# Kernel optimization log

Hardware: AMD Instinct MI355X
Metric: run time of the kernel (lower is better)

## Reference

```python
import jax, jax.numpy as jnp
import numpy as np

B = 32768
NMU = 3
K = 8
TMAX = 31.41592653589793
DE = 128
NC = 64
ZC = 1
IN_DIM = K + K * NMU  # 32

FREQS = jnp.asarray(1.0 / (np.float32(TMAX) ** np.arange(K // 2, dtype=np.float32)))


def _sinenc(x):
    # x: (B,) or (B,d) -> (B, K) or (B, d*K); per-feature [sin|cos] blocks concatenated
    if x.ndim == 1:
        xw = x[:, None] * FREQS[None, :]
        return jnp.concatenate([jnp.sin(xw), jnp.cos(xw)], axis=1)
    xw = x[:, :, None] * FREQS[None, None, :]  # (B, d, K/2)
    return jnp.concatenate([jnp.sin(xw), jnp.cos(xw)], axis=2).reshape(x.shape[0], -1)


def _conv3(x, w, b):
    y = jax.lax.conv_general_dilated(x, w, window_strides=(1, 1), padding=((1, 1), (1, 1)),
                                     dimension_numbers=("NCHW", "OIHW", "NCHW"))
    return y + b[None, :, None, None]


def setup_inputs() -> dict:
    key = jax.random.key(0)
    ks = jax.random.split(key, 20)
    s = 0.05
    return {
        "t": jax.random.uniform(ks[0], (B,), jnp.float32) * TMAX,
        "z": jax.random.normal(ks[1], (B, ZC, 4, 4), jnp.float32),
        "mu": jax.random.normal(ks[2], (B, NMU), jnp.float32),
        "W1": jax.random.normal(ks[3], (IN_DIM, DE), jnp.float32) * s,
        "b1": jnp.zeros((DE,), jnp.float32),
        "W2": jax.random.normal(ks[4], (DE, DE), jnp.float32) * s,
        "b2": jnp.zeros((DE,), jnp.float32),
        "Wg": jax.random.normal(ks[5], (DE, 4 * NC), jnp.float32) * s,
        "bg": jnp.zeros((4 * NC,), jnp.float32),
        "cin_w": jax.random.normal(ks[6], (NC, ZC, 3, 3), jnp.float32) * s,
        "cin_b": jnp.zeros((NC,), jnp.float32),
        "c1_w": jax.random.normal(ks[7], (NC, NC, 3, 3), jnp.float32) * s,
        "c1_b": jnp.zeros((NC,), jnp.float32),
        "c2_w": jax.random.normal(ks[8], (NC, NC, 3, 3), jnp.float32) * s,
        "c2_b": jnp.zeros((NC,), jnp.float32),
        "cout_w": jax.random.normal(ks[9], (ZC, NC, 3, 3), jnp.float32) * s,
        "cout_b": jnp.zeros((ZC,), jnp.float32),
    }


def reference(t, z, mu, W1, b1, W2, b2, Wg, bg,
              cin_w, cin_b, c1_w, c1_b, c2_w, c2_b, cout_w, cout_b):
    t_emb = _sinenc(t)            # (B, K)
    mu_emb = _sinenc(mu)          # (B, K*nmu)
    x = jnp.concatenate([t_emb, mu_emb], axis=1)  # (B, in_dim)
    h = jax.nn.elu(x @ W1 + b1)
    xi = jax.nn.elu(h @ W2 + b2)
    gb = (xi @ Wg + bg).reshape(-1, 4, NC)
    g1 = gb[:, 0][:, :, None, None]
    g2 = gb[:, 1][:, :, None, None]
    bb1 = gb[:, 2][:, :, None, None]
    bb2 = gb[:, 3][:, :, None, None]
    hh = jnp.tanh(_conv3(z, cin_w, cin_b))
    hh = jnp.tanh(g1 * _conv3(hh, c1_w, c1_b) + bb1)
    hh = jnp.tanh(g2 * _conv3(hh, c2_w, c2_b) + bb2)
    return _conv3(hh, cout_w, cout_b)
```

## Files before the change

### kernel.cpp

```cpp
#include <hip/hip_runtime.h>
#include <cstdint>
#include <cstddef>


#define NB 32768

typedef _Float16 half8   __attribute__((ext_vector_type(8)));
typedef _Float16 half4_t __attribute__((ext_vector_type(4)));
typedef _Float16 half2_t __attribute__((ext_vector_type(2)));
typedef float    f32x4   __attribute__((ext_vector_type(4)));

__device__ __forceinline__ float fast_tanh(float x) {
  float e = __expf(2.0f * x);
  return 1.0f - __fdividef(2.0f, e + 1.0f);
}

__device__ __forceinline__ float elu_f(float v) {
  return v > 0.0f ? v : (__expf(v) - 1.0f);
}

__device__ __forceinline__ void conv_acc(float acc[16], const float r[16], const float w[9]) {
#pragma unroll
  for (int y = 0; y < 4; ++y)
#pragma unroll
    for (int x = 0; x < 4; ++x)
#pragma unroll
      for (int ky = 0; ky < 3; ++ky) {
        int iy = y + ky - 1;
        if (iy < 0 || iy >= 4) continue;
#pragma unroll
        for (int kx = 0; kx < 3; ++kx) {
          int ix = x + kx - 1;
          if (ix < 0 || ix >= 4) continue;
          acc[y * 4 + x] += w[ky * 3 + kx] * r[iy * 4 + ix];
        }
      }
}

__global__ __launch_bounds__(256) void prep_kernel(
    const float* __restrict__ W1, const float* __restrict__ W2,
    const float* __restrict__ Wg, const float* __restrict__ c1w,
    const float* __restrict__ c2w, _Float16* __restrict__ wt) {
  int idx = blockIdx.x * 256 + threadIdx.x;
  _Float16* W1f = wt;
  _Float16* W2f = W1f + 4096;
  _Float16* Wgf = W2f + 16384;
  _Float16* c1t = Wgf + 32768;
  _Float16* c2t = c1t + 36864;
  if (idx < 4096) {
    int i = idx, j = i & 7, lane = (i >> 3) & 63, nt = i >> 9;
    int n = nt * 16 + (lane & 15), k = (lane >> 4) * 8 + j;
    W1f[i] = (_Float16)W1[k * 128 + n];
  } else if (idx < 20480) {
    int i = idx - 4096, j = i & 7, lane = (i >> 3) & 63, r = i >> 9;
    int kb = r & 3, nt = r >> 2;
    int n = nt * 16 + (lane & 15), k = kb * 32 + (lane >> 4) * 8 + j;
    W2f[i] = (_Float16)W2[k * 128 + n];
  } else if (idx < 53248) {
    int i = idx - 20480, j = i & 7, lane = (i >> 3) & 63, r = i >> 9;
    int kb = r & 3, ut = r >> 2;
    int n = ut * 16 + (lane & 15), k = kb * 32 + (lane >> 4) * 8 + j;
    Wgf[i] = (_Float16)Wg[k * 256 + n];
  } else if (idx < 90112) {
    int i = idx - 53248;
    int ts = i >> 11, r = i & 2047, oc = r >> 5, icw = r & 31;
    int tap = ts >> 1, kb = ts & 1, ic = kb * 32 + icw;
    c1t[i] = (_Float16)c1w[(oc * 64 + ic) * 9 + tap];
  } else if (idx < 126976) {
    int i = idx - 90112;
    int ts = i >> 11, r = i & 2047, oc = r >> 5, icw = r & 31;
    int tap = ts >> 1, kb = ts & 1, ic = kb * 32 + icw;
    c2t[i] = (_Float16)c2w[(oc * 64 + ic) * 9 + tap];
  }
}

#define ROWE 72
#define SAMP 2592
#define GS 4
#define GRPS 16
#define GBROW 264

__device__ __forceinline__ void mid_layer_mfma(
    const _Float16* __restrict__ src, _Float16* __restrict__ dst,
    const half8 af[18], const f32x4 cbv,
    const _Float16* __restrict__ gbase, int goff,
    int wv, int q, int py, int px) {
  f32x4 acc[GS];
#pragma unroll
  for (int g = 0; g < GS; ++g) acc[g] = (f32x4)(0.0f);
#pragma unroll
  for (int tap = 0; tap < 9; ++tap) {
    const int ky = tap / 3, kx = tap % 3;
    const int row = py + ky;
    const int pos = row * 6 + px + kx;
    const int e = (row ^ (pos >> 2)) & 1;
    const int o0 = pos * ROWE + q * 8 + e * 32;
    const int o1 = pos * ROWE + q * 8 + 32 - e * 32;
#pragma unroll
    for (int g = 0; g < GS; ++g) {
      half8 bb = *(const half8*)(src + g * SAMP + o0);
      acc[g] = __builtin_amdgcn_mfma_f32_16x16x32_f16(af[tap * 2 + 0], bb, acc[g], 0, 0, 0);
    }
#pragma unroll
    for (int g = 0; g < GS; ++g) {
      half8 bb = *(const half8*)(src + g * SAMP + o1);
      acc[g] = __builtin_amdgcn_mfma_f32_16x16x32_f16(af[tap * 2 + 1], bb, acc[g], 0, 0, 0);
    }
  }
  const int icb = wv * 16 + q * 4;
  const int row = 1 + py;
  const int pos = row * 6 + 1 + px;
  const int e = (row ^ (pos >> 2)) & 1;
  const int daddr = pos * ROWE + (((icb >> 5) ^ e) << 5) + (icb & 31);
#pragma unroll
  for (int g = 0; g < GS; ++g) {
    const _Float16* gp = gbase + g * GBROW + goff + icb;
    half4_t gv = *(const half4_t*)(gp);
    half4_t bv = *(const half4_t*)(gp + 128);
    half4_t o;
#pragma unroll
    for (int r = 0; r < 4; ++r)
      o[r] = (_Float16)fast_tanh((float)gv[r] * (acc[g][r] + cbv[r]) + (float)bv[r]);
    *(half4_t*)(dst + g * SAMP + daddr) = o;
  }
}

__global__ __launch_bounds__(256, 2) void fused_kernel(
    const float* __restrict__ tt, const float* __restrict__ mu,
    const float* __restrict__ z, const _Float16* __restrict__ wt,
    const float* __restrict__ b1, const float* __restrict__ b2,
    const float* __restrict__ bg,
    const float* __restrict__ cin_w, const float* __restrict__ cin_b,
    const float* __restrict__ c1_b, const float* __restrict__ c2_b,
    const float* __restrict__ cout_w, const float* __restrict__ cout_b,
    float* __restrict__ out) {
  const int tid = threadIdx.x;
  const int lane = tid & 63;
  const int wv = tid >> 6;
  const int m = lane & 15, q = lane >> 4, q8 = q * 8, q4 = q * 4;
  const int py = m >> 2, px = m & 3;
  const int s0 = blockIdx.x * (GRPS * GS);

  const _Float16* W1f = wt;
  const _Float16* W2f = W1f + 4096;
  const _Float16* Wgf = W2f + 16384;
  const _Float16* c1t = Wgf + 32768;
  const _Float16* c2t = c1t + 36864;

  __shared__ __align__(16) _Float16 hp[2 * GS * SAMP];
  __shared__ __align__(16) _Float16 gb_lds[64 * GBROW];
  __shared__ __align__(16) _Float16 cwl[9 * 64];

  {
    const int sl = wv * 16 + m;
    const int s = s0 + sl;
    _Float16* xw = hp + wv * SAMP;

    const float TM = 31.41592653589793f;
    float base = (q == 0) ? tt[s] : mu[(size_t)s * 3 + (q - 1)];
    half8 xb;
    float fr = 1.0f;
#pragma unroll
    for (int j = 0; j < 4; ++j) {
      float sn, cs;
      __sincosf(base * fr, &sn, &cs);
      xb[j] = (_Float16)sn;
      xb[4 + j] = (_Float16)cs;
      fr *= (1.0f / TM);
    }

#pragma unroll
    for (int nt = 0; nt < 8; ++nt) {
      half8 af = *(const half8*)(W1f + (nt * 64 + lane) * 8);
      f32x4 c = __builtin_amdgcn_mfma_f32_16x16x32_f16(af, xb, (f32x4)(0.0f), 0, 0, 0);
      f32x4 bv = *(const f32x4*)(b1 + nt * 16 + q4);
      half4_t o;
#pragma unroll
      for (int r = 0; r < 4; ++r) o[r] = (_Float16)elu_f(c[r] + bv[r]);
      *(half4_t*)(xw + m * 136 + nt * 16 + q4) = o;
    }
    half8 xf0 = *(const half8*)(xw + m * 136 + 0 + q8);
    half8 xf1 = *(const half8*)(xw + m * 136 + 32 + q8);
    half8 xf2 = *(const half8*)(xw + m * 136 + 64 + q8);
    half8 xf3 = *(const half8*)(xw + m * 136 + 96 + q8);

#pragma unroll
    for (int nt = 0; nt < 8; ++nt) {
      const _Float16* wp = W2f + (nt * 4) * 512 + lane * 8;
      f32x4 c = (f32x4)(0.0f);
      c = __builtin_amdgcn_mfma_f32_16x16x32_f16(*(const half8*)(wp), xf0, c, 0, 0, 0);
      c = __builtin_amdgcn_mfma_f32_16x16x32_f16(*(const half8*)(wp + 512), xf1, c, 0, 0, 0);
      c = __builtin_amdgcn_mfma_f32_16x16x32_f16(*(const half8*)(wp + 1024), xf2, c, 0, 0, 0);
      c = __builtin_amdgcn_mfma_f32_16x16x32_f16(*(const half8*)(wp + 1536), xf3, c, 0, 0, 0);
      f32x4 bv = *(const f32x4*)(b2 + nt * 16 + q4);
      half4_t o;
#pragma unroll
      for (int r = 0; r < 4; ++r) o[r] = (_Float16)elu_f(c[r] + bv[r]);
      *(half4_t*)(xw + m * 136 + nt * 16 + q4) = o;
    }
    half8 yf0 = *(const half8*)(xw + m * 136 + 0 + q8);
    half8 yf1 = *(const half8*)(xw + m * 136 + 32 + q8);
    half8 yf2 = *(const half8*)(xw + m * 136 + 64 + q8);
    half8 yf3 = *(const half8*)(xw + m * 136 + 96 + q8);

#pragma unroll
    for (int ut = 0; ut < 16; ++ut) {
      const _Float16* wp = Wgf + (ut * 4) * 512 + lane * 8;
      f32x4 c = (f32x4)(0.0f);
      c = __builtin_amdgcn_mfma_f32_16x16x32_f16(*(const half8*)(wp), yf0, c, 0, 0, 0);
      c = __builtin_amdgcn_mfma_f32_16x16x32_f16(*(const half8*)(wp + 512), yf1, c, 0, 0, 0);
      c = __builtin_amdgcn_mfma_f32_16x16x32_f16(*(const half8*)(wp + 1024), yf2, c, 0, 0, 0);
      c = __builtin_amdgcn_mfma_f32_16x16x32_f16(*(const half8*)(wp + 1536), yf3, c, 0, 0, 0);
      f32x4 bv = *(const f32x4*)(bg + ut * 16 + q4);
      half4_t o;
#pragma unroll
      for (int r = 0; r < 4; ++r) o[r] = (_Float16)(c[r] + bv[r]);
      *(half4_t*)(gb_lds + sl * GBROW + ut * 16 + q4) = o;
    }
  }

  half8 a1f[18], a2f[18];
#pragma unroll
  for (int t = 0; t < 18; ++t) {
    a1f[t] = *(const half8*)(c1t + t * 2048 + (wv * 16 + m) * 32 + q8);
    a2f[t] = *(const half8*)(c2t + t * 2048 + (wv * 16 + m) * 32 + q8);
  }
  float cw9[9];
#pragma unroll
  for (int t = 0; t < 9; ++t) cw9[t] = cin_w[lane * 9 + t];
  const float cinb = cin_b[lane];
  const float cob = cout_b[0];
  const f32x4 cb1 = *(const f32x4*)(c1_b + wv * 16 + q4);
  const f32x4 cb2 = *(const f32x4*)(c2_b + wv * 16 + q4);

  __syncthreads();

  for (int i = tid; i < (2 * GS * SAMP) / 2; i += 256) ((uint32_t*)hp)[i] = 0u;
  for (int i = tid; i < 576; i += 256) {
    int ic = i / 9, tap = i % 9;
    cwl[tap * 64 + ic] = (_Float16)cout_w[i];
  }
  __syncthreads();

  for (int grp = 0; grp < GRPS; ++grp) {
    const int sg = s0 + grp * GS;
    const _Float16* gbase = gb_lds + (size_t)(grp * GS) * GBROW;

    {
      const float* zp = z + (size_t)(sg + wv) * 16;
      float r[16], acc[16];
#pragma unroll
      for (int p = 0; p < 16; ++p) { r[p] = zp[p]; acc[p] = 0.0f; }
      conv_acc(acc, r, cw9);
      _Float16* dst = hp + wv * SAMP;
      const int ics = lane & 31, ich = lane >> 5;
#pragma unroll
      for (int p = 0; p < 16; ++p) {
        int row = 1 + (p >> 2);
        int pos = row * 6 + 1 + (p & 3);
        int e = (row ^ (pos >> 2)) & 1;
        dst[pos * ROWE + ((ich ^ e) << 5) + ics] = (_Float16)fast_tanh(acc[p] + cinb);
      }
    }
    __syncthreads();

    mid_layer_mfma(hp, hp + GS * SAMP, a1f, cb1, gbase, 0, wv, q, py, px);
    __syncthreads();

    mid_layer_mfma(hp + GS * SAMP, hp, a2f, cb2, gbase, 64, wv, q, py, px);
    __syncthreads();

    {
      const _Float16* src = hp + wv * SAMP;
      const int c32 = q >> 1;
      const int coff = (q * 16) & 31;
      float acc = 0.0f;
#pragma unroll
      for (int tap = 0; tap < 9; ++tap) {
        const int ky = tap / 3, kx = tap % 3;
        const int row = py + ky;
        const int pos = row * 6 + px + kx;
        const int e = (row ^ (pos >> 2)) & 1;
        const _Float16* sp = src + pos * ROWE + ((c32 ^ e) << 5) + coff;
        half8 hv0 = *(const half8*)(sp);
        half8 hv1 = *(const half8*)(sp + 8);
        half8 wv0 = *(const half8*)(cwl + tap * 64 + q * 16);
        half8 wv1 = *(const half8*)(cwl + tap * 64 + q * 16 + 8);
#pragma unroll
        for (int j = 0; j < 4; ++j) {
          half2_t h2a = {hv0[2 * j], hv0[2 * j + 1]};
          half2_t w2a = {wv0[2 * j], wv0[2 * j + 1]};
          half2_t h2b = {hv1[2 * j], hv1[2 * j + 1]};
          half2_t w2b = {wv1[2 * j], wv1[2 * j + 1]};
#if __has_builtin(__builtin_amdgcn_fdot2)
          acc = __builtin_amdgcn_fdot2(h2a, w2a, acc, false);
          acc = __builtin_amdgcn_fdot2(h2b, w2b, acc, false);
#else
          acc += (float)h2a[0] * (float)w2a[0] + (float)h2a[1] * (float)w2a[1];
          acc += (float)h2b[0] * (float)w2b[0] + (float)h2b[1] * (float)w2b[1];
#endif
        }
      }
      acc += __shfl_xor(acc, 16);
      acc += __shfl_xor(acc, 32);
      if (q == 0) out[(size_t)(sg + wv) * 16 + m] = acc + cob;
    }
    __syncthreads();
  }
}

extern "C" void kernel_launch(void* const* d_in, const int* in_sizes, int n_in,
                              void* d_out, int out_size, void* d_ws, size_t ws_size,
                              hipStream_t stream) {
  const float* tt     = (const float*)d_in[0];
  const float* z      = (const float*)d_in[1];
  const float* mu     = (const float*)d_in[2];
  const float* W1     = (const float*)d_in[3];
  const float* b1     = (const float*)d_in[4];
  const float* W2     = (const float*)d_in[5];
  const float* b2     = (const float*)d_in[6];
  const float* Wg     = (const float*)d_in[7];
  const float* bg     = (const float*)d_in[8];
  const float* cin_w  = (const float*)d_in[9];
  const float* cin_b  = (const float*)d_in[10];
  const float* c1_w   = (const float*)d_in[11];
  const float* c1_b   = (const float*)d_in[12];
  const float* c2_w   = (const float*)d_in[13];
  const float* c2_b   = (const float*)d_in[14];
  const float* cout_w = (const float*)d_in[15];
  const float* cout_b = (const float*)d_in[16];

  float* out = (float*)d_out;
  _Float16* wt = (_Float16*)d_ws;

  prep_kernel<<<496, 256, 0, stream>>>(W1, W2, Wg, c1_w, c2_w, wt);
  fused_kernel<<<NB / (GRPS * GS), 256, 0, stream>>>(
      tt, mu, z, wt, b1, b2, bg, cin_w, cin_b, c1_b, c2_b, cout_w, cout_b, out);
}
```

Before: 226.6 us.

## Warp-specialize conv layers into two pipelined wave groups with 32x32 MFMA

The block grows to 512 threads and is split into two wave groups. The first group runs cin and conv1 for the current 4-sample group while the second runs conv2 and cout for the previous group, with double-buffered LDS slots. The mid convolutions switch from 16x16x32 to 32x32x16 MFMA, and conv weights are re-laid out in the prep kernel to match. Each wave now holds only one layer's weights in registers (36 half8), which frees register pressure. In exchange it uses a larger LDS footprint, adds a pipeline fill step, and may leave the two groups with unequal work.

```diff
diff --git a/kernel.cpp b/kernel.cpp
--- a/kernel.cpp
+++ b/kernel.cpp
@@ -9,6 +9,7 @@
 typedef _Float16 half4_t __attribute__((ext_vector_type(4)));
 typedef _Float16 half2_t __attribute__((ext_vector_type(2)));
 typedef float    f32x4   __attribute__((ext_vector_type(4)));
+typedef float    f32x16  __attribute__((ext_vector_type(16)));
 
 __device__ __forceinline__ float fast_tanh(float x) {
   float e = __expf(2.0f * x);
@@ -63,69 +64,74 @@
     Wgf[i] = (_Float16)Wg[k * 256 + n];
   } else if (idx < 90112) {
     int i = idx - 53248;
-    int ts = i >> 11, r = i & 2047, oc = r >> 5, icw = r & 31;
-    int tap = ts >> 1, kb = ts & 1, ic = kb * 32 + icw;
+    int j = i & 7, lane = (i >> 3) & 63, ts = i >> 9;
+    int wtile = ts & 1, f = ts >> 1, kb = f & 3, tap = f >> 2;
+    int oc = wtile * 32 + (lane & 31);
+    int ic = kb * 16 + (lane >> 5) * 8 + j;
     c1t[i] = (_Float16)c1w[(oc * 64 + ic) * 9 + tap];
   } else if (idx < 126976) {
     int i = idx - 90112;
-    int ts = i >> 11, r = i & 2047, oc = r >> 5, icw = r & 31;
-    int tap = ts >> 1, kb = ts & 1, ic = kb * 32 + icw;
+    int j = i & 7, lane = (i >> 3) & 63, ts = i >> 9;
+    int wtile = ts & 1, f = ts >> 1, kb = f & 3, tap = f >> 2;
+    int oc = wtile * 32 + (lane & 31);
+    int ic = kb * 16 + (lane >> 5) * 8 + j;
     c2t[i] = (_Float16)c2w[(oc * 64 + ic) * 9 + tap];
   }
 }
 
 #define ROWE 72
 #define SAMP 2592
-#define GS 4
+#define SLOT (4 * SAMP)
 #define GRPS 16
 #define GBROW 264
 
-__device__ __forceinline__ void mid_layer_mfma(
+__device__ __forceinline__ void mid32(
     const _Float16* __restrict__ src, _Float16* __restrict__ dst,
-    const half8 af[18], const f32x4 cbv,
-    const _Float16* __restrict__ gbase, int goff,
-    int wv, int q, int py, int px) {
-  f32x4 acc[GS];
-#pragma unroll
-  for (int g = 0; g < GS; ++g) acc[g] = (f32x4)(0.0f);
+    const half8 af[36], const f32x4 cb[4],
+    const _Float16* __restrict__ grow, int goff,
+    int wtile, int sp, int lane) {
+  const int col = lane & 31, hi = lane >> 5;
+  const int px = col & 15, sw = col >> 4;
+  const int py = px >> 2, pxx = px & 3;
+  const int samp = sp * 2 + sw;
+  const _Float16* sbase = src + samp * SAMP;
+
+  f32x16 acc = (f32x16)(0.0f);
 #pragma unroll
   for (int tap = 0; tap < 9; ++tap) {
     const int ky = tap / 3, kx = tap % 3;
     const int row = py + ky;
-    const int pos = row * 6 + px + kx;
+    const int pos = row * 6 + pxx + kx;
     const int e = (row ^ (pos >> 2)) & 1;
-    const int o0 = pos * ROWE + q * 8 + e * 32;
-    const int o1 = pos * ROWE + q * 8 + 32 - e * 32;
-#pragma unroll
-    for (int g = 0; g < GS; ++g) {
-      half8 bb = *(const half8*)(src + g * SAMP + o0);
-      acc[g] = __builtin_amdgcn_mfma_f32_16x16x32_f16(af[tap * 2 + 0], bb, acc[g], 0, 0, 0);
-    }
-#pragma unroll
-    for (int g = 0; g < GS; ++g) {
-      half8 bb = *(const half8*)(src + g * SAMP + o1);
-      acc[g] = __builtin_amdgcn_mfma_f32_16x16x32_f16(af[tap * 2 + 1], bb, acc[g], 0, 0, 0);
-    }
-  }
-  const int icb = wv * 16 + q * 4;
-  const int row = 1 + py;
-  const int pos = row * 6 + 1 + px;
-  const int e = (row ^ (pos >> 2)) & 1;
-  const int daddr = pos * ROWE + (((icb >> 5) ^ e) << 5) + (icb & 31);
-#pragma unroll
-  for (int g = 0; g < GS; ++g) {
-    const _Float16* gp = gbase + g * GBROW + goff + icb;
-    half4_t gv = *(const half4_t*)(gp);
-    half4_t bv = *(const half4_t*)(gp + 128);
+#pragma unroll
+    for (int kb = 0; kb < 4; ++kb) {
+      const int ic0 = kb * 16 + hi * 8;
+      const int off = pos * ROWE + ((((ic0 >> 5) ^ e) << 5)) + (ic0 & 31);
+      half8 b = *(const half8*)(sbase + off);
+      acc = __builtin_amdgcn_mfma_f32_32x32x16_f16(af[tap * 4 + kb], b, acc, 0, 0, 0);
+    }
+  }
+
+  const int row_i = 1 + py;
+  const int pos_i = row_i * 6 + 1 + pxx;
+  const int e_i = (row_i ^ (pos_i >> 2)) & 1;
+  _Float16* dbase = dst + samp * SAMP + pos_i * ROWE + ((wtile ^ e_i) << 5);
+  const _Float16* gp = grow + samp * GBROW + goff;
+#pragma unroll
+  for (int g4 = 0; g4 < 4; ++g4) {
+    const int ocb = 8 * g4 + 4 * hi;
+    const int oc = wtile * 32 + ocb;
+    half4_t gv = *(const half4_t*)(gp + oc);
+    half4_t bv = *(const half4_t*)(gp + 128 + oc);
     half4_t o;
 #pragma unroll
     for (int r = 0; r < 4; ++r)
-      o[r] = (_Float16)fast_tanh((float)gv[r] * (acc[g][r] + cbv[r]) + (float)bv[r]);
-    *(half4_t*)(dst + g * SAMP + daddr) = o;
-  }
-}
-
-__global__ __launch_bounds__(256, 2) void fused_kernel(
+      o[r] = (_Float16)fast_tanh((float)gv[r] * (acc[4 * g4 + r] + cb[g4][r]) + (float)bv[r]);
+    *(half4_t*)(dbase + ocb) = o;
+  }
+}
+
+__global__ __launch_bounds__(512, 2) void fused_kernel(
     const float* __restrict__ tt, const float* __restrict__ mu,
     const float* __restrict__ z, const _Float16* __restrict__ wt,
     const float* __restrict__ b1, const float* __restrict__ b2,
@@ -136,10 +142,12 @@
     float* __restrict__ out) {
   const int tid = threadIdx.x;
   const int lane = tid & 63;
-  const int wv = tid >> 6;
-  const int m = lane & 15, q = lane >> 4, q8 = q * 8, q4 = q * 4;
-  const int py = m >> 2, px = m & 3;
-  const int s0 = blockIdx.x * (GRPS * GS);
+  const int wid = tid >> 6;
+  const bool isC2 = (wid >= 4);
+  const int w4 = wid & 3;
+  const int wtile = w4 & 1;
+  const int sp = w4 >> 1;
+  const int s0 = blockIdx.x * (GRPS * 4);
 
   const _Float16* W1f = wt;
   const _Float16* W2f = W1f + 4096;
@@ -147,14 +155,45 @@
   const _Float16* c1t = Wgf + 32768;
   const _Float16* c2t = c1t + 36864;
 
-  __shared__ __align__(16) _Float16 hp[2 * GS * SAMP];
+  __shared__ __align__(16) _Float16 hp[4 * SLOT];
   __shared__ __align__(16) _Float16 gb_lds[64 * GBROW];
   __shared__ __align__(16) _Float16 cwl[9 * 64];
 
-  {
-    const int sl = wv * 16 + m;
+  const int m = lane & 15, q = lane >> 4, q8 = q * 8, q4 = q * 4;
+  const int py16 = m >> 2, px16 = m & 3;
+
+  const _Float16* at = isC2 ? c2t : c1t;
+  half8 af[36];
+#pragma unroll
+  for (int f = 0; f < 36; ++f)
+    af[f] = *(const half8*)(at + ((f * 2 + wtile) << 9) + lane * 8);
+
+  const float* cbsrc = isC2 ? c2_b : c1_b;
+  f32x4 cbv[4];
+#pragma unroll
+  for (int g4 = 0; g4 < 4; ++g4)
+    cbv[g4] = *(const f32x4*)(cbsrc + wtile * 32 + 8 * g4 + 4 * (lane >> 5));
+
+  float cw9[9];
+  float cinb = 0.0f;
+  if (!isC2) {
+#pragma unroll
+    for (int t = 0; t < 9; ++t) cw9[t] = cin_w[lane * 9 + t];
+    cinb = cin_b[lane];
+  } else {
+    for (int i = tid - 256; i < 576; i += 256) {
+      if (i >= 0) {
+        int ic = i / 9, tap = i % 9;
+        cwl[tap * 64 + ic] = (_Float16)cout_w[i];
+      }
+    }
+  }
+  const float cob = cout_b[0];
+
+  if (!isC2) {
+    const int sl = wid * 16 + m;
     const int s = s0 + sl;
-    _Float16* xw = hp + wv * SAMP;
+    _Float16* xw = hp + wid * SAMP;
 
     const float TM = 31.41592653589793f;
     float base = (q == 0) ? tt[s] : mu[(size_t)s * 3 + (q - 1)];
@@ -171,8 +210,8 @@
 
 #pragma unroll
     for (int nt = 0; nt < 8; ++nt) {
-      half8 af = *(const half8*)(W1f + (nt * 64 + lane) * 8);
-      f32x4 c = __builtin_amdgcn_mfma_f32_16x16x32_f16(af, xb, (f32x4)(0.0f), 0, 0, 0);
+      half8 a = *(const half8*)(W1f + (nt * 64 + lane) * 8);
+      f32x4 c = __builtin_amdgcn_mfma_f32_16x16x32_f16(a, xb, (f32x4)(0.0f), 0, 0, 0);
       f32x4 bv = *(const f32x4*)(b1 + nt * 16 + q4);
       half4_t o;
 #pragma unroll
@@ -218,92 +257,83 @@
       *(half4_t*)(gb_lds + sl * GBROW + ut * 16 + q4) = o;
     }
   }
-
-  half8 a1f[18], a2f[18];
-#pragma unroll
-  for (int t = 0; t < 18; ++t) {
-    a1f[t] = *(const half8*)(c1t + t * 2048 + (wv * 16 + m) * 32 + q8);
-    a2f[t] = *(const half8*)(c2t + t * 2048 + (wv * 16 + m) * 32 + q8);
-  }
-  float cw9[9];
-#pragma unroll
-  for (int t = 0; t < 9; ++t) cw9[t] = cin_w[lane * 9 + t];
-  const float cinb = cin_b[lane];
-  const float cob = cout_b[0];
-  const f32x4 cb1 = *(const f32x4*)(c1_b + wv * 16 + q4);
-  const f32x4 cb2 = *(const f32x4*)(c2_b + wv * 16 + q4);
-
   __syncthreads();
 
-  for (int i = tid; i < (2 * GS * SAMP) / 2; i += 256) ((uint32_t*)hp)[i] = 0u;
-  for (int i = tid; i < 576; i += 256) {
-    int ic = i / 9, tap = i % 9;
-    cwl[tap * 64 + ic] = (_Float16)cout_w[i];
+  {
+    uint32_t* hp32 = (uint32_t*)hp;
+    for (int i = tid; i < (4 * SLOT) / 2; i += 512) hp32[i] = 0u;
   }
   __syncthreads();
 
-  for (int grp = 0; grp < GRPS; ++grp) {
-    const int sg = s0 + grp * GS;
-    const _Float16* gbase = gb_lds + (size_t)(grp * GS) * GBROW;
-
-    {
-      const float* zp = z + (size_t)(sg + wv) * 16;
-      float r[16], acc[16];
-#pragma unroll
-      for (int p = 0; p < 16; ++p) { r[p] = zp[p]; acc[p] = 0.0f; }
-      conv_acc(acc, r, cw9);
-      _Float16* dst = hp + wv * SAMP;
-      const int ics = lane & 31, ich = lane >> 5;
-#pragma unroll
-      for (int p = 0; p < 16; ++p) {
-        int row = 1 + (p >> 2);
-        int pos = row * 6 + 1 + (p & 3);
-        int e = (row ^ (pos >> 2)) & 1;
-        dst[pos * ROWE + ((ich ^ e) << 5) + ics] = (_Float16)fast_tanh(acc[p] + cinb);
+  for (int it = 0; it <= GRPS; ++it) {
+    if (!isC2) {
+      if (it < GRPS) {
+        const float* zp = z + (size_t)(s0 + it * 4 + w4) * 16;
+        float r[16], acc[16];
+#pragma unroll
+        for (int p = 0; p < 16; ++p) { r[p] = zp[p]; acc[p] = 0.0f; }
+        conv_acc(acc, r, cw9);
+        _Float16* dst = hp + (it & 1) * SLOT + w4 * SAMP;
+        const int ics = lane & 31, ich = lane >> 5;
+#pragma unroll
+        for (int p = 0; p < 16; ++p) {
+          int row = 1 + (p >> 2);
+          int pos = row * 6 + 1 + (p & 3);
+          int e = (row ^ (pos >> 2)) & 1;
+          dst[pos * ROWE + ((ich ^ e) << 5) + ics] = (_Float16)fast_tanh(acc[p] + cinb);
+        }
+      }
+    } else {
+      if (it >= 1) {
+        const int j = (it - 1) & 1;
+        mid32(hp + (2 + j) * SLOT, hp + j * SLOT, af, cbv,
+              gb_lds + (size_t)((it - 1) * 4) * GBROW, 64, wtile, sp, lane);
       }
     }
     __syncthreads();
 
-    mid_layer_mfma(hp, hp + GS * SAMP, a1f, cb1, gbase, 0, wv, q, py, px);
-    __syncthreads();
-
-    mid_layer_mfma(hp + GS * SAMP, hp, a2f, cb2, gbase, 64, wv, q, py, px);
-    __syncthreads();
-
-    {
-      const _Float16* src = hp + wv * SAMP;
-      const int c32 = q >> 1;
-      const int coff = (q * 16) & 31;
-      float acc = 0.0f;
-#pragma unroll
-      for (int tap = 0; tap < 9; ++tap) {
-        const int ky = tap / 3, kx = tap % 3;
-        const int row = py + ky;
-        const int pos = row * 6 + px + kx;
-        const int e = (row ^ (pos >> 2)) & 1;
-        const _Float16* sp = src + pos * ROWE + ((c32 ^ e) << 5) + coff;
-        half8 hv0 = *(const half8*)(sp);
-        half8 hv1 = *(const half8*)(sp + 8);
-        half8 wv0 = *(const half8*)(cwl + tap * 64 + q * 16);
-        half8 wv1 = *(const half8*)(cwl + tap * 64 + q * 16 + 8);
-#pragma unroll
-        for (int j = 0; j < 4; ++j) {
-          half2_t h2a = {hv0[2 * j], hv0[2 * j + 1]};
-          half2_t w2a = {wv0[2 * j], wv0[2 * j + 1]};
-          half2_t h2b = {hv1[2 * j], hv1[2 * j + 1]};
-          half2_t w2b = {wv1[2 * j], wv1[2 * j + 1]};
+    if (!isC2) {
+      if (it < GRPS) {
+        const int j = it & 1;
+        mid32(hp + j * SLOT, hp + (2 + j) * SLOT, af, cbv,
+              gb_lds + (size_t)(it * 4) * GBROW, 0, wtile, sp, lane);
+      }
+    } else {
+      if (it >= 1) {
+        const _Float16* src = hp + ((it - 1) & 1) * SLOT + w4 * SAMP;
+        const int c32 = q >> 1;
+        const int coff = (q * 16) & 31;
+        float acc = 0.0f;
+#pragma unroll
+        for (int tap = 0; tap < 9; ++tap) {
+          const int ky = tap / 3, kx = tap % 3;
+          const int row = py16 + ky;
+          const int pos = row * 6 + px16 + kx;
+          const int e = (row ^ (pos >> 2)) & 1;
+          const _Float16* spp = src + pos * ROWE + ((c32 ^ e) << 5) + coff;
+          half8 hv0 = *(const half8*)(spp);
+          half8 hv1 = *(const half8*)(spp + 8);
+          half8 wv0 = *(const half8*)(cwl + tap * 64 + q * 16);
+          half8 wv1 = *(const half8*)(cwl + tap * 64 + q * 16 + 8);
+#pragma unroll
+          for (int jj = 0; jj < 4; ++jj) {
+            half2_t h2a = {hv0[2 * jj], hv0[2 * jj + 1]};
+            half2_t w2a = {wv0[2 * jj], wv0[2 * jj + 1]};
+            half2_t h2b = {hv1[2 * jj], hv1[2 * jj + 1]};
+            half2_t w2b = {wv1[2 * jj], wv1[2 * jj + 1]};
 #if __has_builtin(__builtin_amdgcn_fdot2)
-          acc = __builtin_amdgcn_fdot2(h2a, w2a, acc, false);
-          acc = __builtin_amdgcn_fdot2(h2b, w2b, acc, false);
+            acc = __builtin_amdgcn_fdot2(h2a, w2a, acc, false);
+            acc = __builtin_amdgcn_fdot2(h2b, w2b, acc, false);
 #else
-          acc += (float)h2a[0] * (float)w2a[0] + (float)h2a[1] * (float)w2a[1];
-          acc += (float)h2b[0] * (float)w2b[0] + (float)h2b[1] * (float)w2b[1];
+            acc += (float)h2a[0] * (float)w2a[0] + (float)h2a[1] * (float)w2a[1];
+            acc += (float)h2b[0] * (float)w2b[0] + (float)h2b[1] * (float)w2b[1];
 #endif
+          }
         }
-      }
-      acc += __shfl_xor(acc, 16);
-      acc += __shfl_xor(acc, 32);
-      if (q == 0) out[(size_t)(sg + wv) * 16 + m] = acc + cob;
+        acc += __shfl_xor(acc, 16);
+        acc += __shfl_xor(acc, 32);
+        if (q == 0) out[(size_t)(s0 + (it - 1) * 4 + w4) * 16 + m] = acc + cob;
+      }
     }
     __syncthreads();
   }
@@ -334,6 +364,6 @@
   _Float16* wt = (_Float16*)d_ws;
 
   prep_kernel<<<496, 256, 0, stream>>>(W1, W2, Wg, c1_w, c2_w, wt);
-  fused_kernel<<<NB / (GRPS * GS), 256, 0, stream>>>(
+  fused_kernel<<<NB / 64, 512, 0, stream>>>(
       tt, mu, z, wt, b1, b2, bg, cin_w, cin_b, c1_b, c2_b, cout_w, cout_b, out);
 }
```

Measured after the change: 269.2 us. +18.8%, slower.
